# Kernel optimization log

Hardware: AMD Instinct MI355X
Metric: run time of the kernel (lower is better)

Reference implementation:

```python
import jax, jax.numpy as jnp
import numpy as np

B, P, H, W = 64, 50000, 512, 512


def setup_inputs() -> dict:
    key = jax.random.key(0)
    ks = jax.random.split(key, 6)
    x = jax.random.normal(ks[0], (B, 1, H, W), dtype=jnp.float32)
    x_A = jax.random.randint(ks[1], (B, P), 0, W, dtype=jnp.int32)
    y_A = jax.random.randint(ks[2], (B, P), 0, H, dtype=jnp.int32)
    x_B = jax.random.randint(ks[3], (B, P), 0, W, dtype=jnp.int32)
    y_B = jax.random.randint(ks[4], (B, P), 0, H, dtype=jnp.int32)
    # ordinal relation in {-1, 0, 1}: -1/+1 = ordered pair, 0 = equal depth
    gt = jax.random.randint(ks[5], (B, P), -1, 2).astype(jnp.float32)
    return {"x": x, "x_A": x_A, "y_A": y_A, "x_B": x_B, "y_B": y_B, "gt": gt}


def reference(x, x_A, y_A, x_B, y_B, gt):
    # x: [B,1,H,W] predicted depth; gather z values at sparse point pairs.
    img = x[:, 0]                              # [B,H,W]
    b = jnp.arange(B)[:, None]                 # [B,1] batch index for gather
    z_A = img[b, y_A, x_A]                     # [B,P]
    z_B = img[b, y_B, x_B]                     # [B,P]
    d = z_A - z_B
    mask = jnp.abs(gt)                         # 1 for ordered pairs, 0 for equal
    # ranking loss log(1+exp(-gt*d)) for ordered pairs, (d)^2 for equal pairs
    loss = mask * jnp.log1p(jnp.exp(-gt * d)) + (1.0 - mask) * d * d
    n_point_total = B * P
    return jnp.sum(loss) / n_point_total
```

## Files before the change

### kernel.cpp

```cpp
#include <hip/hip_runtime.h>

#define THREADS 1024
#define PPT 16
#define CPB (THREADS * PPT)
#define NCHUNK 4
#define NBANDS 16
#define BAND_F (32 * 512)

__global__ __launch_bounds__(THREADS, 4) void rdc_kernel(
    const float* __restrict__ x,
    const int*   __restrict__ xA,
    const int*   __restrict__ yA,
    const int*   __restrict__ xB,
    const int*   __restrict__ yB,
    const float* __restrict__ gt,
    float* __restrict__ out,
    float inv_n)
{
    __shared__ float band[BAND_F];
    __shared__ float wsum[THREADS / 64];

    const int tid = threadIdx.x;
    const int xcd = blockIdx.x & 7;
    const int w   = blockIdx.x >> 3;
    const int bl  = w >> 2;
    const int ch  = w & 3;
    const int b   = xcd * 8 + bl;
    const int base = ch * CPB;
    const int cnt  = min(CPB, 50000 - base);

    const size_t pbase = (size_t)b * 50000 + base;

    unsigned pa[PPT], pb[PPT];
    float g[PPT], zA[PPT], zB[PPT];
    #pragma unroll
    for (int k = 0; k < PPT; ++k) {
        const int s = k * THREADS + tid;
        if (s < cnt) {
            const size_t p = pbase + s;
            const int xa_ = __builtin_nontemporal_load(xA + p);
            const int ya_ = __builtin_nontemporal_load(yA + p);
            const int xb_ = __builtin_nontemporal_load(xB + p);
            const int yb_ = __builtin_nontemporal_load(yB + p);
            g[k]  = __builtin_nontemporal_load(gt + p);
            pa[k] = (unsigned)((ya_ << 9) | xa_);
            pb[k] = (unsigned)((yb_ << 9) | xb_);
        } else {
            pa[k] = 0xFFFFFFFFu; pb[k] = 0xFFFFFFFFu; g[k] = 0.0f;
        }
        zA[k] = 0.0f; zB[k] = 0.0f;
    }

    const float4* __restrict__ img4 = (const float4*)(x + (size_t)b * (512 * 512));

    for (int bi = 0; bi < NBANDS; ++bi) {
        __syncthreads();
        float4* dst4 = (float4*)band;
        #pragma unroll
        for (int j = 0; j < BAND_F / 4 / THREADS; ++j)
            dst4[j * THREADS + tid] = img4[bi * (BAND_F / 4) + j * THREADS + tid];
        __syncthreads();
        #pragma unroll
        for (int k = 0; k < PPT; ++k) {
            if ((pa[k] >> 14) == (unsigned)bi) zA[k] = band[pa[k] & 16383];
            if ((pb[k] >> 14) == (unsigned)bi) zB[k] = band[pb[k] & 16383];
        }
    }

    float acc = 0.0f;
    #pragma unroll
    for (int k = 0; k < PPT; ++k) {
        const float d = zA[k] - zB[k];
        const float t = -g[k] * d;
        const float sp = fmaxf(t, 0.0f) + log1pf(__expf(-fabsf(t)));
        const float m  = fabsf(g[k]);
        acc += m * sp + (1.0f - m) * d * d;
    }

    #pragma unroll
    for (int off = 32; off > 0; off >>= 1)
        acc += __shfl_down(acc, off, 64);
    const int lane = tid & 63, wid = tid >> 6;
    if (lane == 0) wsum[wid] = acc;
    __syncthreads();
    if (tid == 0) {
        float s = 0.0f;
        #pragma unroll
        for (int i = 0; i < THREADS / 64; ++i) s += wsum[i];
        atomicAdd(out, s * inv_n);
    }
}

extern "C" void kernel_launch(void* const* d_in, const int* in_sizes, int n_in,
                              void* d_out, int out_size, void* d_ws, size_t ws_size,
                              hipStream_t stream) {
    const float* x  = (const float*)d_in[0];
    const int*   xA = (const int*)d_in[1];
    const int*   yA = (const int*)d_in[2];
    const int*   xB = (const int*)d_in[3];
    const int*   yB = (const int*)d_in[4];
    const float* gt = (const float*)d_in[5];
    float* out = (float*)d_out;

    const int n = in_sizes[1];
    const float inv_n = 1.0f / (float)n;

    hipMemsetAsync(out, 0, sizeof(float), stream);
    rdc_kernel<<<64 * NCHUNK, THREADS, 0, stream>>>(x, xA, yA, xB, yB, gt, out, inv_n);
}
```

Before: 188.2 us.

## Double-buffer image bands in LDS and balance points evenly across chunks

Image band staging now uses two LDS buffers. The next band is prefetched into registers while the current band is gathered, which drops one barrier per band and hides global load latency. Points are split evenly, 12500 per block with 13 per thread, instead of 16384-sized chunks that left the last chunk short, so the work is balanced. LDS use doubles to 128KB per block, which limits occupancy to one block per CU, and the launch bound hint is removed.

```diff
diff --git a/kernel.cpp b/kernel.cpp
--- a/kernel.cpp
+++ b/kernel.cpp
@@ -1,13 +1,12 @@
 #include <hip/hip_runtime.h>
 
 #define THREADS 1024
-#define PPT 16
-#define CPB (THREADS * PPT)
-#define NCHUNK 4
+#define PPT 13
+#define QPB 12500
 #define NBANDS 16
-#define BAND_F (32 * 512)
+#define BAND_F 16384
 
-__global__ __launch_bounds__(THREADS, 4) void rdc_kernel(
+__global__ __launch_bounds__(THREADS) void rdc_kernel(
     const float* __restrict__ x,
     const int*   __restrict__ xA,
     const int*   __restrict__ yA,
@@ -17,7 +16,7 @@
     float* __restrict__ out,
     float inv_n)
 {
-    __shared__ float band[BAND_F];
+    __shared__ float buf[2][BAND_F];
     __shared__ float wsum[THREADS / 64];
 
     const int tid = threadIdx.x;
@@ -26,17 +25,21 @@
     const int bl  = w >> 2;
     const int ch  = w & 3;
     const int b   = xcd * 8 + bl;
-    const int base = ch * CPB;
-    const int cnt  = min(CPB, 50000 - base);
 
-    const size_t pbase = (size_t)b * 50000 + base;
+    const size_t pbase = (size_t)b * 50000 + ch * QPB;
+    const float4* __restrict__ img4 = (const float4*)(x + (size_t)b * (512 * 512));
+
+    float4 st[4];
+    #pragma unroll
+    for (int j = 0; j < 4; ++j)
+        st[j] = img4[j * THREADS + tid];
 
     unsigned pa[PPT], pb[PPT];
     float g[PPT], zA[PPT], zB[PPT];
     #pragma unroll
     for (int k = 0; k < PPT; ++k) {
         const int s = k * THREADS + tid;
-        if (s < cnt) {
+        if (s < QPB) {
             const size_t p = pbase + s;
             const int xa_ = __builtin_nontemporal_load(xA + p);
             const int ya_ = __builtin_nontemporal_load(yA + p);
@@ -51,27 +54,40 @@
         zA[k] = 0.0f; zB[k] = 0.0f;
     }
 
-    const float4* __restrict__ img4 = (const float4*)(x + (size_t)b * (512 * 512));
+    {
+        float4* d4 = (float4*)buf[0];
+        #pragma unroll
+        for (int j = 0; j < 4; ++j)
+            d4[j * THREADS + tid] = st[j];
+    }
+    __syncthreads();
 
     for (int bi = 0; bi < NBANDS; ++bi) {
-        __syncthreads();
-        float4* dst4 = (float4*)band;
-        #pragma unroll
-        for (int j = 0; j < BAND_F / 4 / THREADS; ++j)
-            dst4[j * THREADS + tid] = img4[bi * (BAND_F / 4) + j * THREADS + tid];
-        __syncthreads();
+        if (bi + 1 < NBANDS) {
+            #pragma unroll
+            for (int j = 0; j < 4; ++j)
+                st[j] = img4[(bi + 1) * (BAND_F / 4) + j * THREADS + tid];
+        }
+        const float* lb = buf[bi & 1];
         #pragma unroll
         for (int k = 0; k < PPT; ++k) {
-            if ((pa[k] >> 14) == (unsigned)bi) zA[k] = band[pa[k] & 16383];
-            if ((pb[k] >> 14) == (unsigned)bi) zB[k] = band[pb[k] & 16383];
+            if ((pa[k] >> 14) == (unsigned)bi) zA[k] = lb[pa[k] & 16383];
+            if ((pb[k] >> 14) == (unsigned)bi) zB[k] = lb[pb[k] & 16383];
         }
+        if (bi + 1 < NBANDS) {
+            float4* d4 = (float4*)buf[(bi + 1) & 1];
+            #pragma unroll
+            for (int j = 0; j < 4; ++j)
+                d4[j * THREADS + tid] = st[j];
+        }
+        __syncthreads();
     }
 
     float acc = 0.0f;
     #pragma unroll
     for (int k = 0; k < PPT; ++k) {
-        const float d = zA[k] - zB[k];
-        const float t = -g[k] * d;
+        const float d  = zA[k] - zB[k];
+        const float t  = -g[k] * d;
         const float sp = fmaxf(t, 0.0f) + log1pf(__expf(-fabsf(t)));
         const float m  = fabsf(g[k]);
         acc += m * sp + (1.0f - m) * d * d;
@@ -106,5 +122,5 @@
     const float inv_n = 1.0f / (float)n;
 
     hipMemsetAsync(out, 0, sizeof(float), stream);
-    rdc_kernel<<<64 * NCHUNK, THREADS, 0, stream>>>(x, xA, yA, xB, yB, gt, out, inv_n);
+    rdc_kernel<<<256, THREADS, 0, stream>>>(x, xA, yA, xB, yB, gt, out, inv_n);
 }
```

After: 176.7 us. -6.1%, faster.
